# Kernel tuning notes

Hardware: AMD Instinct MI355X
Metric: run time of the kernel (lower is better)

Reference implementation:

```python
import jax, jax.numpy as jnp
import numpy as np

EPS_NORM = 1e-12
EPS_LOG = 1e-10


def _l2norm(x):
    # F.normalize(x, dim=-1): x / max(||x||, 1e-12)
    n = jnp.sqrt(jnp.sum(x * x, axis=-1, keepdims=True))
    return x / jnp.maximum(n, EPS_NORM)


def setup_inputs() -> dict:
    key = jax.random.key(0)
    k1, k2 = jax.random.split(key)
    N, K, D = 524288, 256, 128
    z_e = jax.random.normal(k1, (N, D), dtype=jnp.float32)
    # xavier_uniform init for [K, D] codebook
    bound = float(np.sqrt(6.0 / (K + D)))
    embeddings = jax.random.uniform(k2, (K, D), dtype=jnp.float32, minval=-bound, maxval=bound)
    logit_scale = jnp.ones((1,), dtype=jnp.float32) * 10.0
    return {"z_e": z_e, "embeddings": embeddings, "logit_scale": logit_scale}


def reference(z_e, embeddings, logit_scale):
    z_n = _l2norm(z_e)                         # [N, D]
    e_n = _l2norm(embeddings)                  # [K, D]
    logits = logit_scale * jnp.einsum('nd,kd->nk', z_n, e_n)  # [N, K] cosine sims
    indices = jnp.argmax(logits, axis=-1)      # [N]
    z_q = embeddings[indices]                  # [N, D] gather
    probs = jax.nn.softmax(logits, axis=-1)    # [N, K]
    avg_probs = probs.mean(axis=0)             # [K]
    perplexity = jnp.exp(-jnp.sum(avg_probs * jnp.log(avg_probs + EPS_LOG)))
    return (z_q, indices, perplexity)
```

## Files before the change

kernel.cpp:

```cpp
#include <hip/hip_runtime.h>
#include <cmath>

#define NTOT 524288
#define KC   256
#define DD   128

__global__ __launch_bounds__(64) void vq_prep(const float* __restrict__ emb,
                                              float* __restrict__ et,
                                              float* __restrict__ pacc_g) {
  const int c = blockIdx.x;
  const int l = threadIdx.x;
  const float a = emb[c * DD + l];
  const float b = emb[c * DD + 64 + l];
  float s = a * a + b * b;
#pragma unroll
  for (int m = 32; m >= 1; m >>= 1) s += __shfl_xor(s, m, 64);
  const float inv = 1.0f / fmaxf(sqrtf(s), 1e-12f);
  et[l * KC + c] = a * inv;
  et[(l + 64) * KC + c] = b * inv;
  if (l == 0) pacc_g[c] = 0.0f;
}

__global__ __launch_bounds__(256, 4) void vq_main(
    const float* __restrict__ z, const float* __restrict__ emb,
    const float* __restrict__ et, const float* __restrict__ lsp,
    float* __restrict__ zq, float* __restrict__ oidx, float* __restrict__ pacc_g) {
  __shared__ __align__(16) float zt[16][68];
  __shared__ float nrm2[64];
  __shared__ float pp[KC];

  const int t    = threadIdx.x;
  const int tx   = t & 31;
  const int ty   = t >> 5;
  const int srow = t >> 2;
  const int sq   = t & 3;
  const int lane = t & 63;
  const int halfbase = lane & 32;

  const float lscale = lsp[0];

  float pacc[8];
#pragma unroll
  for (int j = 0; j < 8; ++j) pacc[j] = 0.0f;

  for (int tile = blockIdx.x; tile < (NTOT / 64); tile += gridDim.x) {
    const int r0 = tile * 64;
    float acc[8][8];
#pragma unroll
    for (int i = 0; i < 8; ++i)
#pragma unroll
      for (int j = 0; j < 8; ++j) acc[i][j] = 0.0f;
    float nl = 0.0f;
    if (t < 64) nrm2[t] = 0.0f;

    for (int ch = 0; ch < 8; ++ch) {
      const int d0 = ch * 16;
      const float4 v = *(const float4*)(z + (size_t)(r0 + srow) * DD + d0 + sq * 4);
      nl += v.x * v.x + v.y * v.y + v.z * v.z + v.w * v.w;
      __syncthreads();
      zt[sq * 4 + 0][srow] = v.x;
      zt[sq * 4 + 1][srow] = v.y;
      zt[sq * 4 + 2][srow] = v.z;
      zt[sq * 4 + 3][srow] = v.w;
      __syncthreads();
#pragma unroll
      for (int dd = 0; dd < 16; ++dd) {
        const float4 e0 = *(const float4*)(et + (size_t)(d0 + dd) * KC + tx * 8);
        const float4 e1 = *(const float4*)(et + (size_t)(d0 + dd) * KC + tx * 8 + 4);
        const float4 za = *(const float4*)(&zt[dd][ty * 8]);
        const float4 zb = *(const float4*)(&zt[dd][ty * 8 + 4]);
        const float zr[8] = {za.x, za.y, za.z, za.w, zb.x, zb.y, zb.z, zb.w};
        const float er[8] = {e0.x, e0.y, e0.z, e0.w, e1.x, e1.y, e1.z, e1.w};
#pragma unroll
        for (int i = 0; i < 8; ++i)
#pragma unroll
          for (int j = 0; j < 8; ++j) acc[i][j] = fmaf(zr[i], er[j], acc[i][j]);
      }
    }
    atomicAdd(&nrm2[srow], nl);
    __syncthreads();

#pragma unroll
    for (int i = 0; i < 8; ++i) {
      const int r = r0 + ty * 8 + i;
      const float inv = lscale / fmaxf(sqrtf(nrm2[ty * 8 + i]), 1e-12f);
      float l8[8];
#pragma unroll
      for (int j = 0; j < 8; ++j) l8[j] = acc[i][j] * inv;

      float m1 = l8[0];
      int i1 = tx * 8;
#pragma unroll
      for (int j = 1; j < 8; ++j)
        if (l8[j] > m1) { m1 = l8[j]; i1 = tx * 8 + j; }
#pragma unroll
      for (int s = 16; s >= 1; s >>= 1) {
        const float om = __shfl_xor(m1, s, 64);
        const int   oi = __shfl_xor(i1, s, 64);
        if (om > m1 || (om == m1 && oi < i1)) { m1 = om; i1 = oi; }
      }
      float m2 = -3.0e38f;
      int iy2 = 0;
#pragma unroll
      for (int j = 0; j < 8; ++j) {
        const int c = tx * 8 + j;
        if (c != i1 && l8[j] > m2) { m2 = l8[j]; iy2 = c; }
      }
#pragma unroll
      for (int s = 16; s >= 1; s >>= 1) {
        const float om = __shfl_xor(m2, s, 64);
        const int   oi = __shfl_xor(iy2, s, 64);
        if (om > m2 || (om == m2 && oi < iy2)) { m2 = om; iy2 = oi; }
      }
      if (m1 - m2 < 1.0e-3f) {
        if (tx == 0) {
          const float* e1p = emb + (size_t)i1 * DD;
          const float* e2p = emb + (size_t)iy2 * DD;
          const float* zp  = z + (size_t)r * DD;
          double s1 = 0.0, s2 = 0.0, q1 = 0.0, q2 = 0.0;
#pragma unroll 1
          for (int d = 0; d < DD; ++d) {
            const double zd = zp[d];
            const double a = e1p[d];
            const double b = e2p[d];
            s1 += zd * a; s2 += zd * b; q1 += a * a; q2 += b * b;
          }
          const double v1 = s1 / sqrt(q1);
          const double v2 = s2 / sqrt(q2);
          if (v2 > v1 || (v2 == v1 && iy2 < i1)) i1 = iy2;
        }
        i1 = __shfl(i1, halfbase, 64);
      }
      float se = 0.0f;
      float pr[8];
#pragma unroll
      for (int j = 0; j < 8; ++j) { pr[j] = expf(l8[j] - m1); se += pr[j]; }
#pragma unroll
      for (int s = 16; s >= 1; s >>= 1) se += __shfl_xor(se, s, 64);
      const float rs = 1.0f / se;
#pragma unroll
      for (int j = 0; j < 8; ++j) pacc[j] = fmaf(pr[j], rs, pacc[j]);

      const float4 ev = *(const float4*)(emb + (size_t)i1 * DD + tx * 4);
      *(float4*)(zq + (size_t)r * DD + tx * 4) = ev;
      if (tx == 0) oidx[r] = (float)i1;
    }
    __syncthreads();
  }

  pp[t] = 0.0f;
  __syncthreads();
#pragma unroll
  for (int j = 0; j < 8; ++j) atomicAdd(&pp[tx * 8 + j], pacc[j]);
  __syncthreads();
  atomicAdd(&pacc_g[t], pp[t]);
}

__global__ __launch_bounds__(256) void vq_perp(const float* __restrict__ pacc_g,
                                               float* __restrict__ outp) {
  __shared__ double red[256];
  const int t = threadIdx.x;
  const double p = (double)pacc_g[t] * (1.0 / (double)NTOT);
  red[t] = p * log(p + 1e-10);
  __syncthreads();
  for (int s = 128; s > 0; s >>= 1) {
    if (t < s) red[t] += red[t + s];
    __syncthreads();
  }
  if (t == 0) outp[0] = (float)exp(-red[0]);
}

extern "C" void kernel_launch(void* const* d_in, const int* in_sizes, int n_in,
                              void* d_out, int out_size, void* d_ws, size_t ws_size,
                              hipStream_t stream) {
  const float* z   = (const float*)d_in[0];
  const float* emb = (const float*)d_in[1];
  const float* lsp = (const float*)d_in[2];

  float* ws_probs = (float*)d_ws;
  float* ws_et    = ws_probs + KC;

  float* zq    = (float*)d_out;
  float* oidx  = zq + (size_t)NTOT * DD;
  float* operp = oidx + NTOT;

  vq_prep<<<KC, 64, 0, stream>>>(emb, ws_et, ws_probs);
  vq_main<<<2048, 256, 0, stream>>>(z, emb, ws_et, lsp, zq, oidx, ws_probs);
  vq_perp<<<1, 256, 0, stream>>>(ws_probs, operp);
}
```

Before: 1.313 ms.

## Replace FP32 FMA GEMM with split-bf16 MFMA and per-wave row tiles

Replaces the scalar FP32 outer-product distance GEMM with bf16 MFMA 16x16x32 instructions. It keeps near-FP32 accuracy by splitting both z and the normalized codebook into hi and lo bf16 parts and issuing three MFMAs per product. Each wave now owns a 16-row tile staged in swizzled LDS, which removes block-wide syncthreads. The near-tie fallback is widened to re-check the top three candidates in double precision. The cost is extra conversion work, triple MFMA issue, and a lower occupancy hint.

Measured after the change: 1.597 ms. +21.6%, slower.

```diff
diff --git a/kernel.cpp b/kernel.cpp
--- a/kernel.cpp
+++ b/kernel.cpp
@@ -5,8 +5,21 @@
 #define KC   256
 #define DD   128
 
+typedef __attribute__((ext_vector_type(8))) short bf16x8;
+typedef __attribute__((ext_vector_type(4))) float f32x4;
+
+static __device__ __forceinline__ unsigned short f2bf(float f) {
+  unsigned int u = __float_as_uint(f);
+  u = (u + 0x7fffu + ((u >> 16) & 1u)) >> 16;
+  return (unsigned short)u;
+}
+static __device__ __forceinline__ float bf2f(unsigned short h) {
+  return __uint_as_float(((unsigned int)h) << 16);
+}
+
 __global__ __launch_bounds__(64) void vq_prep(const float* __restrict__ emb,
-                                              float* __restrict__ et,
+                                              unsigned short* __restrict__ ephi,
+                                              unsigned short* __restrict__ eplo,
                                               float* __restrict__ pacc_g) {
   const int c = blockIdx.x;
   const int l = threadIdx.x;
@@ -16,142 +29,185 @@
 #pragma unroll
   for (int m = 32; m >= 1; m >>= 1) s += __shfl_xor(s, m, 64);
   const float inv = 1.0f / fmaxf(sqrtf(s), 1e-12f);
-  et[l * KC + c] = a * inv;
-  et[(l + 64) * KC + c] = b * inv;
+  if (l < 16) {
+#pragma unroll
+    for (int j = 0; j < 8; ++j) {
+      const float v = emb[c * DD + l * 8 + j] * inv;
+      const unsigned short h = f2bf(v);
+      const unsigned short lo = f2bf(v - bf2f(h));
+      const size_t off = ((size_t)l * KC + c) * 8 + j;
+      ephi[off] = h;
+      eplo[off] = lo;
+    }
+  }
   if (l == 0) pacc_g[c] = 0.0f;
 }
 
-__global__ __launch_bounds__(256, 4) void vq_main(
+__global__ __launch_bounds__(256, 2) void vq_main(
     const float* __restrict__ z, const float* __restrict__ emb,
-    const float* __restrict__ et, const float* __restrict__ lsp,
+    const unsigned short* __restrict__ ephi, const unsigned short* __restrict__ eplo,
+    const float* __restrict__ lsp,
     float* __restrict__ zq, float* __restrict__ oidx, float* __restrict__ pacc_g) {
-  __shared__ __align__(16) float zt[16][68];
-  __shared__ float nrm2[64];
+  __shared__ __align__(16) char zplds[32768];
+  __shared__ float nrm[4][16];
   __shared__ float pp[KC];
 
-  const int t    = threadIdx.x;
-  const int tx   = t & 31;
-  const int ty   = t >> 5;
-  const int srow = t >> 2;
-  const int sq   = t & 3;
-  const int lane = t & 63;
-  const int halfbase = lane & 32;
+  const int t  = threadIdx.x;
+  const int w  = t >> 6;
+  const int l  = t & 63;
+  const int lg = l >> 4;
+  const int lx = l & 15;
 
   const float lscale = lsp[0];
-
-  float pacc[8];
-#pragma unroll
-  for (int j = 0; j < 8; ++j) pacc[j] = 0.0f;
-
-  for (int tile = blockIdx.x; tile < (NTOT / 64); tile += gridDim.x) {
-    const int r0 = tile * 64;
-    float acc[8][8];
-#pragma unroll
-    for (int i = 0; i < 8; ++i)
-#pragma unroll
-      for (int j = 0; j < 8; ++j) acc[i][j] = 0.0f;
-    float nl = 0.0f;
-    if (t < 64) nrm2[t] = 0.0f;
-
-    for (int ch = 0; ch < 8; ++ch) {
-      const int d0 = ch * 16;
-      const float4 v = *(const float4*)(z + (size_t)(r0 + srow) * DD + d0 + sq * 4);
-      nl += v.x * v.x + v.y * v.y + v.z * v.z + v.w * v.w;
-      __syncthreads();
-      zt[sq * 4 + 0][srow] = v.x;
-      zt[sq * 4 + 1][srow] = v.y;
-      zt[sq * 4 + 2][srow] = v.z;
-      zt[sq * 4 + 3][srow] = v.w;
-      __syncthreads();
-#pragma unroll
-      for (int dd = 0; dd < 16; ++dd) {
-        const float4 e0 = *(const float4*)(et + (size_t)(d0 + dd) * KC + tx * 8);
-        const float4 e1 = *(const float4*)(et + (size_t)(d0 + dd) * KC + tx * 8 + 4);
-        const float4 za = *(const float4*)(&zt[dd][ty * 8]);
-        const float4 zb = *(const float4*)(&zt[dd][ty * 8 + 4]);
-        const float zr[8] = {za.x, za.y, za.z, za.w, zb.x, zb.y, zb.z, zb.w};
-        const float er[8] = {e0.x, e0.y, e0.z, e0.w, e1.x, e1.y, e1.z, e1.w};
-#pragma unroll
-        for (int i = 0; i < 8; ++i)
-#pragma unroll
-          for (int j = 0; j < 8; ++j) acc[i][j] = fmaf(zr[i], er[j], acc[i][j]);
-      }
-    }
-    atomicAdd(&nrm2[srow], nl);
-    __syncthreads();
-
-#pragma unroll
-    for (int i = 0; i < 8; ++i) {
-      const int r = r0 + ty * 8 + i;
-      const float inv = lscale / fmaxf(sqrtf(nrm2[ty * 8 + i]), 1e-12f);
-      float l8[8];
-#pragma unroll
-      for (int j = 0; j < 8; ++j) l8[j] = acc[i][j] * inv;
-
-      float m1 = l8[0];
-      int i1 = tx * 8;
-#pragma unroll
-      for (int j = 1; j < 8; ++j)
-        if (l8[j] > m1) { m1 = l8[j]; i1 = tx * 8 + j; }
-#pragma unroll
-      for (int s = 16; s >= 1; s >>= 1) {
+  char* const zpw_hi = zplds + w * 8192;
+  char* const zpw_lo = zpw_hi + 4096;
+  const bf16x8* const ebhi = (const bf16x8*)ephi;
+  const bf16x8* const eblo = (const bf16x8*)eplo;
+
+  float pacc[16];
+#pragma unroll
+  for (int n = 0; n < 16; ++n) pacc[n] = 0.0f;
+
+  for (int tile = blockIdx.x * 4 + w; tile < (NTOT / 16); tile += gridDim.x * 4) {
+    const int r0 = tile * 16;
+
+#pragma unroll
+    for (int i = 0; i < 4; ++i) {
+      const int row = i * 4 + lg;
+      const int dg  = lx;
+      const float4* zp4 = (const float4*)(z + (size_t)(r0 + row) * DD + dg * 8);
+      const float4 va = zp4[0];
+      const float4 vb = zp4[1];
+      float s = va.x * va.x + va.y * va.y + va.z * va.z + va.w * va.w
+              + vb.x * vb.x + vb.y * vb.y + vb.z * vb.z + vb.w * vb.w;
+#pragma unroll
+      for (int m = 8; m >= 1; m >>= 1) s += __shfl_xor(s, m, 64);
+      if (lx == 0) nrm[w][row] = s;
+      const float vv[8] = {va.x, va.y, va.z, va.w, vb.x, vb.y, vb.z, vb.w};
+      bf16x8 hv, lv;
+#pragma unroll
+      for (int j = 0; j < 8; ++j) {
+        const unsigned short h = f2bf(vv[j]);
+        hv[j] = (short)h;
+        lv[j] = (short)f2bf(vv[j] - bf2f(h));
+      }
+      const int boff = (((dg << 8) + (row << 4))) ^ ((dg & 7) << 4);
+      *(bf16x8*)(zpw_hi + boff) = hv;
+      *(bf16x8*)(zpw_lo + boff) = lv;
+    }
+
+    f32x4 acc[16];
+#pragma unroll
+    for (int n = 0; n < 16; ++n) acc[n] = (f32x4){0.f, 0.f, 0.f, 0.f};
+
+#pragma unroll
+    for (int kc = 0; kc < 4; ++kc) {
+      const int dg = kc * 4 + lg;
+      const int aoff = (((dg << 8) + (lx << 4))) ^ ((dg & 7) << 4);
+      const bf16x8 ahi = *(const bf16x8*)(zpw_hi + aoff);
+      const bf16x8 alo = *(const bf16x8*)(zpw_lo + aoff);
+      const int bbase = dg * 256 + lx;
+#pragma unroll
+      for (int n = 0; n < 16; ++n) {
+        const bf16x8 bhi = ebhi[bbase + n * 16];
+        const bf16x8 blo = eblo[bbase + n * 16];
+        acc[n] = __builtin_amdgcn_mfma_f32_16x16x32_bf16(ahi, bhi, acc[n], 0, 0, 0);
+        acc[n] = __builtin_amdgcn_mfma_f32_16x16x32_bf16(alo, bhi, acc[n], 0, 0, 0);
+        acc[n] = __builtin_amdgcn_mfma_f32_16x16x32_bf16(ahi, blo, acc[n], 0, 0, 0);
+      }
+    }
+
+#pragma unroll
+    for (int r = 0; r < 4; ++r) {
+      const int rowi = lg * 4 + r;
+      const int R = r0 + rowi;
+      const float inv = lscale / fmaxf(sqrtf(nrm[w][rowi]), 1e-12f);
+      float l16[16];
+#pragma unroll
+      for (int n = 0; n < 16; ++n) l16[n] = acc[n][r] * inv;
+
+      float m1 = l16[0]; int i1 = lx;
+#pragma unroll
+      for (int n = 1; n < 16; ++n) {
+        const int c = n * 16 + lx;
+        if (l16[n] > m1) { m1 = l16[n]; i1 = c; }
+      }
+#pragma unroll
+      for (int s = 8; s >= 1; s >>= 1) {
         const float om = __shfl_xor(m1, s, 64);
         const int   oi = __shfl_xor(i1, s, 64);
         if (om > m1 || (om == m1 && oi < i1)) { m1 = om; i1 = oi; }
       }
-      float m2 = -3.0e38f;
-      int iy2 = 0;
-#pragma unroll
-      for (int j = 0; j < 8; ++j) {
-        const int c = tx * 8 + j;
-        if (c != i1 && l8[j] > m2) { m2 = l8[j]; iy2 = c; }
-      }
-#pragma unroll
-      for (int s = 16; s >= 1; s >>= 1) {
+      float m2 = -3.0e38f; int i2 = 0;
+#pragma unroll
+      for (int n = 0; n < 16; ++n) {
+        const int c = n * 16 + lx;
+        if (c != i1 && l16[n] > m2) { m2 = l16[n]; i2 = c; }
+      }
+#pragma unroll
+      for (int s = 8; s >= 1; s >>= 1) {
         const float om = __shfl_xor(m2, s, 64);
-        const int   oi = __shfl_xor(iy2, s, 64);
-        if (om > m2 || (om == m2 && oi < iy2)) { m2 = om; iy2 = oi; }
+        const int   oi = __shfl_xor(i2, s, 64);
+        if (om > m2 || (om == m2 && oi < i2)) { m2 = om; i2 = oi; }
       }
       if (m1 - m2 < 1.0e-3f) {
-        if (tx == 0) {
-          const float* e1p = emb + (size_t)i1 * DD;
-          const float* e2p = emb + (size_t)iy2 * DD;
-          const float* zp  = z + (size_t)r * DD;
-          double s1 = 0.0, s2 = 0.0, q1 = 0.0, q2 = 0.0;
+        float m3 = -3.0e38f; int i3 = 0;
+#pragma unroll
+        for (int n = 0; n < 16; ++n) {
+          const int c = n * 16 + lx;
+          if (c != i1 && c != i2 && l16[n] > m3) { m3 = l16[n]; i3 = c; }
+        }
+#pragma unroll
+        for (int s = 8; s >= 1; s >>= 1) {
+          const float om = __shfl_xor(m3, s, 64);
+          const int   oi = __shfl_xor(i3, s, 64);
+          if (om > m3 || (om == m3 && oi < i3)) { m3 = om; i3 = oi; }
+        }
+        if (lx == 0) {
+          const float* zp = z + (size_t)R * DD;
+          const float* e1 = emb + (size_t)i1 * DD;
+          const float* e2 = emb + (size_t)i2 * DD;
+          const float* e3 = emb + (size_t)i3 * DD;
+          double s1 = 0.0, s2 = 0.0, s3 = 0.0, q1 = 0.0, q2 = 0.0, q3 = 0.0;
 #pragma unroll 1
           for (int d = 0; d < DD; ++d) {
             const double zd = zp[d];
-            const double a = e1p[d];
-            const double b = e2p[d];
-            s1 += zd * a; s2 += zd * b; q1 += a * a; q2 += b * b;
+            const double a1 = e1[d], a2 = e2[d], a3 = e3[d];
+            s1 += zd * a1; q1 += a1 * a1;
+            s2 += zd * a2; q2 += a2 * a2;
+            s3 += zd * a3; q3 += a3 * a3;
           }
           const double v1 = s1 / sqrt(q1);
           const double v2 = s2 / sqrt(q2);
-          if (v2 > v1 || (v2 == v1 && iy2 < i1)) i1 = iy2;
+          const double v3 = s3 / sqrt(q3);
+          double vb = v1; int ib = i1;
+          if (v2 > vb || (v2 == vb && i2 < ib)) { vb = v2; ib = i2; }
+          if (v3 > vb || (v3 == vb && i3 < ib)) { vb = v3; ib = i3; }
+          i1 = ib;
         }
-        i1 = __shfl(i1, halfbase, 64);
-      }
-      float se = 0.0f;
-      float pr[8];
-#pragma unroll
-      for (int j = 0; j < 8; ++j) { pr[j] = expf(l8[j] - m1); se += pr[j]; }
-#pragma unroll
-      for (int s = 16; s >= 1; s >>= 1) se += __shfl_xor(se, s, 64);
+        i1 = __shfl(i1, (l & 48), 64);
+      }
+      float se = 0.0f, pr[16];
+#pragma unroll
+      for (int n = 0; n < 16; ++n) { pr[n] = expf(l16[n] - m1); se += pr[n]; }
+#pragma unroll
+      for (int s = 8; s >= 1; s >>= 1) se += __shfl_xor(se, s, 64);
       const float rs = 1.0f / se;
 #pragma unroll
-      for (int j = 0; j < 8; ++j) pacc[j] = fmaf(pr[j], rs, pacc[j]);
-
-      const float4 ev = *(const float4*)(emb + (size_t)i1 * DD + tx * 4);
-      *(float4*)(zq + (size_t)r * DD + tx * 4) = ev;
-      if (tx == 0) oidx[r] = (float)i1;
-    }
-    __syncthreads();
+      for (int n = 0; n < 16; ++n) pacc[n] = fmaf(pr[n], rs, pacc[n]);
+
+      const float4 e0 = *(const float4*)(emb + (size_t)i1 * DD + lx * 8);
+      const float4 e1v = *(const float4*)(emb + (size_t)i1 * DD + lx * 8 + 4);
+      *(float4*)(zq + (size_t)R * DD + lx * 8) = e0;
+      *(float4*)(zq + (size_t)R * DD + lx * 8 + 4) = e1v;
+      if (lx == 0) oidx[R] = (float)i1;
+    }
   }
 
   pp[t] = 0.0f;
   __syncthreads();
 #pragma unroll
-  for (int j = 0; j < 8; ++j) atomicAdd(&pp[tx * 8 + j], pacc[j]);
+  for (int n = 0; n < 16; ++n) atomicAdd(&pp[n * 16 + lx], pacc[n]);
   __syncthreads();
   atomicAdd(&pacc_g[t], pp[t]);
 }
@@ -178,13 +234,14 @@
   const float* lsp = (const float*)d_in[2];
 
   float* ws_probs = (float*)d_ws;
-  float* ws_et    = ws_probs + KC;
+  unsigned short* ws_ephi = (unsigned short*)(ws_probs + KC);
+  unsigned short* ws_eplo = ws_ephi + 16 * KC * 8;
 
   float* zq    = (float*)d_out;
   float* oidx  = zq + (size_t)NTOT * DD;
   float* operp = oidx + NTOT;
 
-  vq_prep<<<KC, 64, 0, stream>>>(emb, ws_et, ws_probs);
-  vq_main<<<2048, 256, 0, stream>>>(z, emb, ws_et, lsp, zq, oidx, ws_probs);
+  vq_prep<<<KC, 64, 0, stream>>>(emb, ws_ephi, ws_eplo, ws_probs);
+  vq_main<<<2048, 256, 0, stream>>>(z, emb, ws_ephi, ws_eplo, lsp, zq, oidx, ws_probs);
   vq_perp<<<1, 256, 0, stream>>>(ws_probs, operp);
 }
```
